# Kernel tuning notes

Hardware: AMD Instinct MI355X
Metric: run time of the kernel (lower is better)

## Reference

```python
import jax, jax.numpy as jnp
import numpy as np

B, S, H = 4, 2048, 1024
NH, HD = 16, 64
FF = 4096
EPS = 1e-5

def _ln(x, g, b):
    m = jnp.mean(x, axis=-1, keepdims=True)
    v = jnp.var(x, axis=-1, keepdims=True)
    return (x - m) * jax.lax.rsqrt(v + EPS) * g + b

def setup_inputs() -> dict:
    key = jax.random.key(0)
    ks = jax.random.split(key, 12)
    sc = 0.02
    return {
        "hidden_states": jax.random.normal(ks[0], (B, S, H), jnp.float32),
        "Wq": jax.random.normal(ks[1], (H, H), jnp.float32) * sc,
        "bq": jnp.zeros((H,), jnp.float32),
        "Wk": jax.random.normal(ks[2], (H, H), jnp.float32) * sc,
        "bk": jnp.zeros((H,), jnp.float32),
        "Wv": jax.random.normal(ks[3], (H, H), jnp.float32) * sc,
        "bv": jnp.zeros((H,), jnp.float32),
        "Wi": jax.random.normal(ks[4], (H, FF), jnp.float32) * sc,
        "bi": jnp.zeros((FF,), jnp.float32),
        "Wo": jax.random.normal(ks[5], (FF, H), jnp.float32) * sc,
        "bo": jnp.zeros((H,), jnp.float32),
        "g1": jnp.ones((H,), jnp.float32),
        "b1": jnp.zeros((H,), jnp.float32),
        "g2": jnp.ones((H,), jnp.float32),
        "b2": jnp.zeros((H,), jnp.float32),
    }

def reference(hidden_states, Wq, bq, Wk, bk, Wv, bv, Wi, bi, Wo, bo, g1, b1, g2, b2):
    x = hidden_states
    # projections -> [B, NH, S, HD]
    def split(t):
        return t.reshape(B, S, NH, HD).transpose(0, 2, 1, 3)
    q = split(x @ Wq + bq)
    k = split(x @ Wk + bk)
    v = split(x @ Wv + bv)
    scores = jnp.einsum('bhqd,bhkd->bhqk', q, k) / jnp.sqrt(jnp.float32(HD))
    probs = jax.nn.softmax(scores, axis=-1)
    ctx = jnp.einsum('bhqk,bhkd->bhqd', probs, v)
    attn_out = ctx.transpose(0, 2, 1, 3).reshape(B, S, H)
    h = _ln(x + attn_out, g1, b1)
    ffn = jax.nn.gelu(h @ Wi + bi, approximate=False) @ Wo + bo
    return _ln(h + ffn, g2, b2)
```

## Files before the change

kernel.cpp:

```cpp
#include <hip/hip_runtime.h>

#define B_  4
#define S_  2048
#define H_  1024
#define NH_ 16
#define HD_ 64
#define FF_ 4096
#define M_  (B_*S_)

typedef __bf16 bf16x8 __attribute__((ext_vector_type(8)));
typedef float  f32x4  __attribute__((ext_vector_type(4)));
typedef unsigned short ushort8v __attribute__((ext_vector_type(8)));
typedef unsigned short ushort4v __attribute__((ext_vector_type(4)));

typedef __attribute__((address_space(1))) void GVOID;
typedef __attribute__((address_space(3))) void LVOID;

__device__ __forceinline__ void g2l16(const void* g, void* l) {
  __builtin_amdgcn_global_load_lds((GVOID*)g, (LVOID*)l, 16, 0, 0);
}

#define MFMA16(a, b, c) __builtin_amdgcn_mfma_f32_16x16x32_bf16(a, b, c, 0, 0, 0)

#if __has_builtin(__builtin_amdgcn_exp2f)
#define EXP2(x) __builtin_amdgcn_exp2f(x)
#else
#define EXP2(x) exp2f(x)
#endif

__device__ __forceinline__ unsigned short f2bf(float f) {
  unsigned int u = __float_as_uint(f);
  u += 0x7fffu + ((u >> 16) & 1u);
  return (unsigned short)(u >> 16);
}
__device__ __forceinline__ float bf2f(unsigned short h) {
  return __uint_as_float(((unsigned int)h) << 16);
}

__device__ __forceinline__ float gelu_fast(float v) {
  float y = 0.7978845608f * (v + 0.044715f * v * v * v);
  float e = EXP2(y * 2.8853900818f);
  float th = 1.0f - 2.0f / (e + 1.0f);
  return 0.5f * v * (1.0f + th);
}

__device__ __forceinline__ void xcd_swz(int& bx, int& by) {
  int gx = gridDim.x;
  int flat = by * gx + bx;
  int cpx = (gx * gridDim.y) >> 3;
  int swz = (flat & 7) * cpx + (flat >> 3);
  bx = swz % gx;
  by = swz / gx;
}

__device__ __forceinline__ void xcd_swzT(int& bx, int& by) {
  int gy = gridDim.y;
  int flat = bx * gy + by;
  int cpx = (gridDim.x * gy) >> 3;
  int swz = (flat & 7) * cpx + (flat >> 3);
  by = swz % gy;
  bx = swz / gy;
}

__global__ __launch_bounds__(256) void cast_f32_bf16(const float* __restrict__ in,
                                                     unsigned short* __restrict__ out,
                                                     int n4) {
  int i = blockIdx.x * 256 + threadIdx.x;
  if (i >= n4) return;
  float4 v = reinterpret_cast<const float4*>(in)[i];
  ushort4v o;
  o[0] = f2bf(v.x); o[1] = f2bf(v.y); o[2] = f2bf(v.z); o[3] = f2bf(v.w);
  reinterpret_cast<ushort4v*>(out)[i] = o;
}

__global__ __launch_bounds__(256) void prep_weights(const float* __restrict__ Wq,
                                                    const float* __restrict__ Wk,
                                                    const float* __restrict__ Wv,
                                                    const float* __restrict__ Wi,
                                                    const float* __restrict__ Wo,
                                                    unsigned short* __restrict__ WqkvT,
                                                    unsigned short* __restrict__ WiT,
                                                    unsigned short* __restrict__ WoT) {
  __shared__ float t[32][33];
  int id = blockIdx.x;
  const float* in; unsigned short* out; int R, C, bx, by;
  if (id < 3072) {
    int seg = id >> 10, rem = id & 1023;
    in = (seg == 0) ? Wq : (seg == 1) ? Wk : Wv;
    out = WqkvT + (size_t)seg * H_ * H_;
    R = H_; C = H_;
    bx = rem & 31; by = rem >> 5;
  } else if (id < 3072 + 4096) {
    int rem = id - 3072;
    in = Wi; out = WiT; R = H_; C = FF_;
    bx = rem & 127; by = rem >> 7;
  } else {
    int rem = id - 3072 - 4096;
    in = Wo; out = WoT; R = FF_; C = H_;
    bx = rem & 31; by = rem >> 5;
  }
  bx *= 32; by *= 32;
  const int tx = threadIdx.x & 31, ty = threadIdx.x >> 5;
#pragma unroll
  for (int i = 0; i < 32; i += 8)
    t[ty + i][tx] = in[(size_t)(by + ty + i) * C + bx + tx];
  __syncthreads();
#pragma unroll
  for (int i = 0; i < 32; i += 8)
    out[(size_t)(bx + ty + i) * R + by + tx] = f2bf(t[tx][ty + i]);
}

#define ALOAD(bufv, mf, ks)                                                      \
  *reinterpret_cast<const bf16x8*>((char*)As + (bufv)*32768 + wm*16384 +         \
      ((mf)*16 + lr)*128 + (((((ks)*4 + kg)) ^ (lr & 7)) * 16))
#define BLOAD(bufv, nf, ks)                                                      \
  *reinterpret_cast<const bf16x8*>((char*)Bs + (bufv)*32768 + bh*16384 +         \
      (brow0 + (nf)*16 + lr)*128 + (((((ks)*4 + kg)) ^ (lr & 7)) * 16))

#define PH_MFMA(MF0)                                                             \
  __builtin_amdgcn_s_barrier();                                                  \
  asm volatile("s_waitcnt lgkmcnt(0)" ::: "memory");                             \
  __builtin_amdgcn_s_setprio(1);                                                 \
  _Pragma("unroll")                                                              \
  for (int nf = 0; nf < 4; ++nf) {                                               \
    acc[MF0][nf]     = MFMA16(a_[0][0], bfr[nf][0], acc[MF0][nf]);               \
    acc[MF0][nf]     = MFMA16(a_[0][1], bfr[nf][1], acc[MF0][nf]);               \
    acc[MF0 + 1][nf] = MFMA16(a_[1][0], bfr[nf][0], acc[MF0 + 1][nf]);           \
    acc[MF0 + 1][nf] = MFMA16(a_[1][1], bfr[nf][1], acc[MF0 + 1][nf]);           \
  }                                                                              \
  __builtin_amdgcn_s_setprio(0);

#define GEMM256_CORE(A_, Bt_, LDK_, NKT_, KOFF_)                                 \
  __shared__ unsigned short As[2][2][128 * 64];                                  \
  __shared__ unsigned short Bs[2][2][128 * 64];                                  \
  const int tid  = threadIdx.x;                                                  \
  const int wave = tid >> 6;                                                     \
  const int lane = tid & 63;                                                     \
  const int kg   = lane >> 4;                                                    \
  const int lr   = lane & 15;                                                    \
  const int wm   = wave >> 2;                                                    \
  const int wn   = wave & 3;                                                     \
  const int bh   = wn >> 1;                                                      \
  const int brow0 = (wn & 1) * 64;                                               \
  const int sr = lane >> 3;                                                      \
  const int sc = ((lane & 7) ^ sr) * 8;                                          \
  const unsigned short* sA = &A_[(size_t)(m0 + wave * 8 + sr) * LDK_ + KOFF_ + sc];  \
  const unsigned short* sB = &Bt_[(size_t)(n0 + wave * 8 + sr) * LDK_ + KOFF_ + sc]; \
  char* ldsA = (char*)&As[0][0][0] + wave * 1024;                                \
  char* ldsB = (char*)&Bs[0][0][0] + wave * 1024;                                \
  const size_t rkI = (size_t)64 * LDK_;                                          \
  const size_t rhK = (size_t)128 * LDK_;                                         \
  f32x4 acc[8][4] = {};                                                          \
  const int nkt = (NKT_);                                                        \
  g2l16(sA,             ldsA);                                                   \
  g2l16(sA + rkI,       ldsA + 8192);                                            \
  g2l16(sA + rhK,       ldsA + 16384);                                           \
  g2l16(sA + rhK + rkI, ldsA + 16384 + 8192);                                    \
  g2l16(sB,             ldsB);                                                   \
  g2l16(sB + rkI,       ldsB + 8192);                                            \
  g2l16(sB + rhK,       ldsB + 16384);                                           \
  g2l16(sB + rhK + rkI, ldsB + 16384 + 8192);                                    \
  g2l16(sB + 64,             ldsB + 32768);                                      \
  g2l16(sB + rkI + 64,       ldsB + 32768 + 8192);                               \
  g2l16(sB + rhK + 64,       ldsB + 32768 + 16384);                              \
  g2l16(sB + rhK + rkI + 64, ldsB + 32768 + 16384 + 8192);                       \
  asm volatile("s_waitcnt vmcnt(4)" ::: "memory");                               \
  __builtin_amdgcn_s_barrier();                                                  \
  for (int c = 0; c < nkt; ++c) {                                                \
    const int buf = c & 1;                                                       \
    const bool stgA = (c + 1 < nkt);                                             \
    const bool stgB = (c + 2 < nkt);                                             \
    const size_t kA = (size_t)(c + 1) * 64;                                      \
    const size_t kB = (size_t)(c + 2) * 64;                                      \
    bf16x8 bfr[4][2];                                                            \
    bf16x8 a_[2][2];                                                             \
    _Pragma("unroll")                                                            \
    for (int nf = 0; nf < 4; ++nf) {                                             \
      bfr[nf][0] = BLOAD(buf, nf, 0);                                            \
      bfr[nf][1] = BLOAD(buf, nf, 1);                                            \
    }                                                                            \
    a_[0][0] = ALOAD(buf, 0, 0); a_[0][1] = ALOAD(buf, 0, 1);                    \
    a_[1][0] = ALOAD(buf, 1, 0); a_[1][1] = ALOAD(buf, 1, 1);                    \
    if (stgA) {                                                                  \
      g2l16(sA + kA,       ldsA + (buf ^ 1) * 32768);                            \
      g2l16(sA + rkI + kA, ldsA + (buf ^ 1) * 32768 + 8192);                     \
    }                                                                            \
    PH_MFMA(0)                                                                   \
    __builtin_amdgcn_s_barrier();                                                \
    a_[0][0] = ALOAD(buf, 2, 0); a_[0][1] = ALOAD(buf, 2, 1);                    \
    a_[1][0] = ALOAD(buf, 3, 0); a_[1][1] = ALOAD(buf, 3, 1);                    \
    if (stgA) {                                                                  \
      g2l16(sA + rhK + kA,       ldsA + (buf ^ 1) * 32768 + 16384);              \
      g2l16(sA + rhK + rkI + kA, ldsA + (buf ^ 1) * 32768 + 16384 + 8192);       \
    }                                                                            \
    PH_MFMA(2)                                                                   \
    __builtin_amdgcn_s_barrier();                                                \
    a_[0][0] = ALOAD(buf, 4, 0); a_[0][1] = ALOAD(buf, 4, 1);                    \
    a_[1][0] = ALOAD(buf, 5, 0); a_[1][1] = ALOAD(buf, 5, 1);                    \
    if (stgB) {                                                                  \
      g2l16(sB + kB,       ldsB + buf * 32768);                                  \
      g2l16(sB + rkI + kB, ldsB + buf * 32768 + 8192);                           \
    }                                                                            \
    PH_MFMA(4)                                                                   \
    __builtin_amdgcn_s_barrier();                                                \
    a_[0][0] = ALOAD(buf, 6, 0); a_[0][1] = ALOAD(buf, 6, 1);                    \
    a_[1][0] = ALOAD(buf, 7, 0); a_[1][1] = ALOAD(buf, 7, 1);                    \
    if (stgB) {                                                                  \
      g2l16(sB + rhK + kB,       ldsB + buf * 32768 + 16384);                    \
      g2l16(sB + rhK + rkI + kB, ldsB + buf * 32768 + 16384 + 8192);             \
    }                                                                            \
    PH_MFMA(6)                                                                   \
    if (c < nkt - 2)       asm volatile("s_waitcnt vmcnt(4)" ::: "memory");      \
    else if (c == nkt - 2) asm volatile("s_waitcnt vmcnt(0)" ::: "memory");      \
    __builtin_amdgcn_s_barrier();                                                \
  }

template<int ACT, int OUT_F32>
__global__ __launch_bounds__(512, 1) void gemm256_tn(const unsigned short* __restrict__ A,
                                                     const unsigned short* __restrict__ Bt,
                                                     const float* __restrict__ bias,
                                                     void* __restrict__ C,
                                                     int M, int N, int K) {
  int bx = blockIdx.x, by = blockIdx.y;
  xcd_swzT(bx, by);
  const int z = blockIdx.z;
  const int Klen = K / gridDim.z;
  const int Koff = z * Klen;
  const float* biasEff = (z == 0) ? bias : nullptr;
  const int m0 = bx * 256;
  const int n0 = by * 256;
  GEMM256_CORE(A, Bt, K, Klen >> 6, Koff)

  float* Cf = (float*)C + (size_t)z * M * N;
#pragma unroll
  for (int mf = 0; mf < 8; ++mf) {
#pragma unroll
    for (int nf = 0; nf < 4; ++nf) {
      int col = n0 + wn * 64 + nf * 16 + lr;
      float bc = biasEff ? biasEff[col] : 0.0f;
#pragma unroll
      for (int r = 0; r < 4; ++r) {
        int row = m0 + wm * 128 + mf * 16 + kg * 4 + r;
        float v = acc[mf][nf][r] + bc;
        if (ACT == 1) v = gelu_fast(v);
        if (OUT_F32) Cf[(size_t)row * N + col] = v;
        else reinterpret_cast<unsigned short*>(C)[(size_t)row * N + col] = f2bf(v);
      }
    }
  }
}

__global__ __launch_bounds__(512, 1) void gemm256_qkv(const unsigned short* __restrict__ A,
                                                      const unsigned short* __restrict__ Bt,
                                                      const float* __restrict__ bq,
                                                      const float* __restrict__ bk,
                                                      const float* __restrict__ bv,
                                                      unsigned short* __restrict__ qb,
                                                      unsigned short* __restrict__ kb,
                                                      unsigned short* __restrict__ vt,
                                                      float qscale) {
  int bx = blockIdx.x, by = blockIdx.y;
  xcd_swzT(bx, by);
  const int m0 = bx * 256;
  const int n0 = by * 256;
  GEMM256_CORE(A, Bt, H_, H_ >> 6, 0)

#pragma unroll
  for (int mf = 0; mf < 8; ++mf) {
#pragma unroll
    for (int nf = 0; nf < 4; ++nf) {
      int colb = n0 + wn * 64 + nf * 16;
      int col  = colb + lr;
      int seg  = colb >> 10;
      int row0 = m0 + wm * 128 + mf * 16 + kg * 4;
      if (seg == 0) {
        float bc = bq[col];
#pragma unroll
        for (int r = 0; r < 4; ++r)
          qb[(size_t)(row0 + r) * H_ + col] = f2bf((acc[mf][nf][r] + bc) * qscale);
      } else if (seg == 1) {
        float bc = bk[col - 1024];
#pragma unroll
        for (int r = 0; r < 4; ++r)
          kb[(size_t)(row0 + r) * H_ + col - 1024] = f2bf(acc[mf][nf][r] + bc);
      } else {
        float bc = bv[col - 2048];
        ushort4v o;
#pragma unroll
        for (int r = 0; r < 4; ++r) o[r] = f2bf(acc[mf][nf][r] + bc);
        *reinterpret_cast<ushort4v*>(&vt[(size_t)(col - 2048) * M_ + row0]) = o;
      }
    }
  }
}

__global__ __launch_bounds__(512) void attn_fwd(const unsigned short* __restrict__ Q,
                                                const unsigned short* __restrict__ Kb,
                                                const unsigned short* __restrict__ VT,
                                                unsigned short* __restrict__ O) {
  __shared__ unsigned short Ks[2][64 * 64];
  __shared__ unsigned short Vs[2][64 * 64];
  __shared__ __bf16 Ps[8][32 * 64];

  const int tid  = threadIdx.x;
  const int wave = tid >> 6;
  const int lane = tid & 63;
  const int kg   = lane >> 4;
  const int lr   = lane & 15;
  int bx = blockIdx.x, by = blockIdx.y;
  xcd_swz(bx, by);
  const int b  = by >> 4;
  const int h  = by & 15;
  const size_t rowbase = (size_t)b * S_;
  const int hcol = h * 64;
  const int bcol0 = b * S_;
  const int q0 = bx * 256 + wave * 32;

  const int rT = wave * 8 + (lane >> 3);
  const int ce = ((lane & 7) * 8) ^ (((lane >> 3) & 7) << 3);
  const int fswz = (lr & 7) << 3;

  bf16x8 qf[2][2];
#pragma unroll
  for (int sub = 0; sub < 2; ++sub)
#pragma unroll
    for (int d = 0; d < 2; ++d)
      qf[sub][d] = *reinterpret_cast<const bf16x8*>(
          &Q[(rowbase + q0 + sub * 16 + lr) * H_ + hcol + d * 32 + kg * 8]);

  bf16x8 ones;
#pragma unroll
  for (int i = 0; i < 8; ++i) ones[i] = (__bf16)1.0f;

  const f32x4 cinit = {-8.0f, -8.0f, -8.0f, -8.0f};

  f32x4 ctx[2][4] = {};
  f32x4 lsum[2] = {};

  auto stage = [&](int kt, int buf) {
    g2l16(&Kb[(rowbase + kt * 64 + rT) * H_ + hcol + ce], &Ks[buf][wave * 512]);
    g2l16(&VT[(size_t)(hcol + rT) * M_ + bcol0 + kt * 64 + ce], &Vs[buf][wave * 512]);
  };

  stage(0, 0);
  __syncthreads();

  const int NT = S_ / 64;
  for (int kt = 0; kt < NT; ++kt) {
    const int cur = kt & 1;
    if (kt + 1 < NT) stage(kt + 1, cur ^ 1);

    f32x4 s0[4], s1[4];
    __builtin_amdgcn_s_setprio(1);
#pragma unroll
    for (int nf = 0; nf < 4; ++nf) {
      int row = nf * 16 + lr;
      bf16x8 kf0 = *reinterpret_cast<const bf16x8*>(&Ks[cur][row * 64 + ((kg * 8) ^ fswz)]);
      bf16x8 kf1 = *reinterpret_cast<const bf16x8*>(&Ks[cur][row * 64 + ((32 + kg * 8) ^ fswz)]);
      f32x4 z0 = cinit, z1 = cinit;
      z0 = MFMA16(qf[0][0], kf0, z0);
      z0 = MFMA16(qf[0][1], kf1, z0);
      z1 = MFMA16(qf[1][0], kf0, z1);
      z1 = MFMA16(qf[1][1], kf1, z1);
      s0[nf] = z0;
      s1[nf] = z1;
    }
    __builtin_amdgcn_s_setprio(0);

#pragma unroll
    for (int nf = 0; nf < 4; ++nf)
#pragma unroll
      for (int r = 0; r < 4; ++r) {
        int row = kg * 4 + r;
        Ps[wave][row * 64 + ((nf * 16 + lr) ^ ((row & 7) << 3))] =
            (__bf16)EXP2(s0[nf][r]);
        Ps[wave][(16 + row) * 64 + ((nf * 16 + lr) ^ ((row & 7) << 3))] =
            (__bf16)EXP2(s1[nf][r]);
      }
    bf16x8 p00 = *reinterpret_cast<const bf16x8*>(
        &Ps[wave][lr * 64 + ((kg ^ (lr & 7)) << 3)]);
    bf16x8 p01 = *reinterpret_cast<const bf16x8*>(
        &Ps[wave][lr * 64 + (((4 + kg) ^ (lr & 7)) << 3)]);
    bf16x8 p10 = *reinterpret_cast<const bf16x8*>(
        &Ps[wave][(16 + lr) * 64 + ((kg ^ (lr & 7)) << 3)]);
    bf16x8 p11 = *reinterpret_cast<const bf16x8*>(
        &Ps[wave][(16 + lr) * 64 + (((4 + kg) ^ (lr & 7)) << 3)]);

    __builtin_amdgcn_s_setprio(1);
#pragma unroll
    for (int df = 0; df < 4; ++df) {
      int row = df * 16 + lr;
      bf16x8 vf0 = *reinterpret_cast<const bf16x8*>(&Vs[cur][row * 64 + ((kg * 8) ^ fswz)]);
      bf16x8 vf1 = *reinterpret_cast<const bf16x8*>(&Vs[cur][row * 64 + ((32 + kg * 8) ^ fswz)]);
      ctx[0][df] = MFMA16(p00, vf0, ctx[0][df]);
      ctx[0][df] = MFMA16(p01, vf1, ctx[0][df]);
      ctx[1][df] = MFMA16(p10, vf0, ctx[1][df]);
      ctx[1][df] = MFMA16(p11, vf1, ctx[1][df]);
    }
    lsum[0] = MFMA16(p00, ones, lsum[0]);
    lsum[0] = MFMA16(p01, ones, lsum[0]);
    lsum[1] = MFMA16(p10, ones, lsum[1]);
    lsum[1] = MFMA16(p11, ones, lsum[1]);
    __builtin_amdgcn_s_setprio(0);

    __syncthreads();
  }

#pragma unroll
  for (int sub = 0; sub < 2; ++sub)
#pragma unroll
    for (int r = 0; r < 4; ++r) {
      float rl = 1.0f / lsum[sub][r];
#pragma unroll
      for (int df = 0; df < 4; ++df) {
        float v = ctx[sub][df][r] * rl;
        O[(rowbase + q0 + sub * 16 + kg * 4 + r) * H_ + hcol + df * 16 + lr] = f2bf(v);
      }
    }
}

template<int IN2_BF16, int WRITE_BF16>
__global__ __launch_bounds__(256) void add_ln(const float* __restrict__ X,
                                              const void* __restrict__ Y,
                                              const float* __restrict__ g,
                                              const float* __restrict__ beta,
                                              float* __restrict__ outF,
                                              unsigned short* __restrict__ outB) {
  const int row = blockIdx.x;
  const int tid = threadIdx.x;
  const int wave = tid >> 6, lane = tid & 63;
  __shared__ float red[8];

  const size_t base = (size_t)row * H_ + tid * 4;
  float4 xv = *reinterpret_cast<const float4*>(&X[base]);
  float vals[4] = {xv.x, xv.y, xv.z, xv.w};
  if (IN2_BF16) {
    ushort4v yv = *reinterpret_cast<const ushort4v*>(
        &reinterpret_cast<const unsigned short*>(Y)[base]);
#pragma unroll
    for (int i = 0; i < 4; ++i) vals[i] += bf2f(yv[i]);
  } else {
    float4 yv = *reinterpret_cast<const float4*>(&reinterpret_cast<const float*>(Y)[base]);
    vals[0] += yv.x; vals[1] += yv.y; vals[2] += yv.z; vals[3] += yv.w;
  }
  float s = 0.0f, s2 = 0.0f;
#pragma unroll
  for (int i = 0; i < 4; ++i) { s += vals[i]; s2 += vals[i] * vals[i]; }
#pragma unroll
  for (int off = 32; off; off >>= 1) { s += __shfl_xor(s, off); s2 += __shfl_xor(s2, off); }
  if (lane == 0) { red[wave * 2] = s; red[wave * 2 + 1] = s2; }
  __syncthreads();
  s  = red[0] + red[2] + red[4] + red[6];
  s2 = red[1] + red[3] + red[5] + red[7];
  float mean = s * (1.0f / H_);
  float var  = s2 * (1.0f / H_) - mean * mean;
  float rstd = rsqrtf(var + 1e-5f);

  float4 gv = *reinterpret_cast<const float4*>(&g[tid * 4]);
  float4 bv = *reinterpret_cast<const float4*>(&beta[tid * 4]);
  float gs[4] = {gv.x, gv.y, gv.z, gv.w};
  float bs[4] = {bv.x, bv.y, bv.z, bv.w};
  float4 of;
  ushort4v ob;
#pragma unroll
  for (int i = 0; i < 4; ++i) {
    float v = (vals[i] - mean) * rstd * gs[i] + bs[i];
    ((float*)&of)[i] = v;
    ob[i] = f2bf(v);
  }
  if (outF) *reinterpret_cast<float4*>(&outF[base]) = of;
  if (WRITE_BF16) *reinterpret_cast<ushort4v*>(&outB[base]) = ob;
}

__global__ __launch_bounds__(256) void add_ln3(const float* __restrict__ X,
                                               const float* __restrict__ Y0,
                                               const float* __restrict__ Y1,
                                               const float* __restrict__ g,
                                               const float* __restrict__ beta,
                                               float* __restrict__ outF) {
  const int row = blockIdx.x;
  const int tid = threadIdx.x;
  const int wave = tid >> 6, lane = tid & 63;
  __shared__ float red[8];

  const size_t base = (size_t)row * H_ + tid * 4;
  float4 xv = *reinterpret_cast<const float4*>(&X[base]);
  float4 y0 = *reinterpret_cast<const float4*>(&Y0[base]);
  float4 y1 = *reinterpret_cast<const float4*>(&Y1[base]);
  float vals[4] = {xv.x + y0.x + y1.x, xv.y + y0.y + y1.y,
                   xv.z + y0.z + y1.z, xv.w + y0.w + y1.w};
  float s = 0.0f, s2 = 0.0f;
#pragma unroll
  for (int i = 0; i < 4; ++i) { s += vals[i]; s2 += vals[i] * vals[i]; }
#pragma unroll
  for (int off = 32; off; off >>= 1) { s += __shfl_xor(s, off); s2 += __shfl_xor(s2, off); }
  if (lane == 0) { red[wave * 2] = s; red[wave * 2 + 1] = s2; }
  __syncthreads();
  s  = red[0] + red[2] + red[4] + red[6];
  s2 = red[1] + red[3] + red[5] + red[7];
  float mean = s * (1.0f / H_);
  float var  = s2 * (1.0f / H_) - mean * mean;
  float rstd = rsqrtf(var + 1e-5f);

  float4 gv = *reinterpret_cast<const float4*>(&g[tid * 4]);
  float4 bv = *reinterpret_cast<const float4*>(&beta[tid * 4]);
  float4 of;
  of.x = (vals[0] - mean) * rstd * gv.x + bv.x;
  of.y = (vals[1] - mean) * rstd * gv.y + bv.y;
  of.z = (vals[2] - mean) * rstd * gv.z + bv.z;
  of.w = (vals[3] - mean) * rstd * gv.w + bv.w;
  *reinterpret_cast<float4*>(&outF[base]) = of;
}

extern "C" void kernel_launch(void* const* d_in, const int* in_sizes, int n_in,
                              void* d_out, int out_size, void* d_ws, size_t ws_size,
                              hipStream_t stream) {
  const float* x  = (const float*)d_in[0];
  const float* Wq = (const float*)d_in[1];
  const float* bq = (const float*)d_in[2];
  const float* Wk = (const float*)d_in[3];
  const float* bk = (const float*)d_in[4];
  const float* Wv = (const float*)d_in[5];
  const float* bv = (const float*)d_in[6];
  const float* Wi = (const float*)d_in[7];
  const float* bi = (const float*)d_in[8];
  const float* Wo = (const float*)d_in[9];
  const float* bo = (const float*)d_in[10];
  const float* g1 = (const float*)d_in[11];
  const float* b1 = (const float*)d_in[12];
  const float* g2 = (const float*)d_in[13];
  const float* b2 = (const float*)d_in[14];

  unsigned char* ws = (unsigned char*)d_ws;
  size_t off = 0;
  auto alloc = [&](size_t bytes) { size_t o = off; off += (bytes + 255) & ~(size_t)255; return o; };

  unsigned short* WqkvT = (unsigned short*)(ws + alloc((size_t)3 * H_ * H_ * 2));
  unsigned short* WiT   = (unsigned short*)(ws + alloc((size_t)H_ * FF_ * 2));
  unsigned short* WoT   = (unsigned short*)(ws + alloc((size_t)FF_ * H_ * 2));
  float*          hf    = (float*)(ws + alloc((size_t)M_ * H_ * 4));
  unsigned short* hb    = (unsigned short*)(ws + alloc((size_t)M_ * H_ * 2));
  unsigned short* f1    = (unsigned short*)(ws + alloc((size_t)M_ * FF_ * 2));
  unsigned short* xb    = (unsigned short*)(ws + alloc((size_t)M_ * H_ * 2));
  unsigned short* qb    = (unsigned short*)(ws + alloc((size_t)M_ * H_ * 2));
  unsigned short* kb    = (unsigned short*)(ws + alloc((size_t)M_ * H_ * 2));
  unsigned short* vt    = (unsigned short*)(ws + alloc((size_t)M_ * H_ * 2));
  unsigned short* ao    = (unsigned short*)(ws + alloc((size_t)M_ * H_ * 2));
  float*          f2p   = (float*)xb;

  {
    int n4 = (int)((size_t)M_ * H_ / 4);
    cast_f32_bf16<<<(n4 + 255) / 256, 256, 0, stream>>>(x, xb, n4);
  }
  prep_weights<<<3072 + 4096 + 4096, 256, 0, stream>>>(Wq, Wk, Wv, Wi, Wo,
                                                       WqkvT, WiT, WoT);

  const float QSCALE = 0.125f * 1.44269504088896340736f;

  gemm256_qkv<<<dim3(M_ / 256, 3072 / 256), 512, 0, stream>>>(xb, WqkvT, bq, bk, bv,
                                                              qb, kb, vt, QSCALE);

  attn_fwd<<<dim3(S_ / 256, B_ * NH_), 512, 0, stream>>>(qb, kb, vt, ao);

  add_ln<1, 1><<<M_, 256, 0, stream>>>(x, ao, g1, b1, hf, hb);

  gemm256_tn<1, 0><<<dim3(M_ / 256, FF_ / 256), 512, 0, stream>>>(hb, WiT, bi, f1, M_, FF_, H_);
  gemm256_tn<0, 1><<<dim3(M_ / 256, H_ / 256, 2), 512, 0, stream>>>(f1, WoT, bo, f2p, M_, H_, FF_);

  add_ln3<<<M_, 256, 0, stream>>>(hf, f2p, f2p + (size_t)M_ * H_, g2, b2, (float*)d_out);
}
```

Measured before the change: 433.5 us.

## Compute transposed scores in attention to keep P in registers; drop fp32 LN1 output

The attention kernel now computes S^T by swapping MFMA operands. Each lane then holds probabilities along keys, and the P fragments for the PV MFMA are assembled with cross-lane shuffles instead of a round trip through LDS. Row sums come from in-register adds plus shuffles rather than extra MFMAs against a ones vector, and the output is written as packed 4-element vectors. Separately, the first LayerNorm writes only a bf16 output, and the second residual reads that bf16 tensor, removing an fp32 M×H write and read at some cost in residual precision.

```diff
diff --git a/kernel.cpp b/kernel.cpp
--- a/kernel.cpp
+++ b/kernel.cpp
@@ -12,6 +12,7 @@
 typedef float  f32x4  __attribute__((ext_vector_type(4)));
 typedef unsigned short ushort8v __attribute__((ext_vector_type(8)));
 typedef unsigned short ushort4v __attribute__((ext_vector_type(4)));
+typedef unsigned int   uint4v   __attribute__((ext_vector_type(4)));
 
 typedef __attribute__((address_space(1))) void GVOID;
 typedef __attribute__((address_space(3))) void LVOID;
@@ -300,7 +301,6 @@
                                                 unsigned short* __restrict__ O) {
   __shared__ unsigned short Ks[2][64 * 64];
   __shared__ unsigned short Vs[2][64 * 64];
-  __shared__ __bf16 Ps[8][32 * 64];
 
   const int tid  = threadIdx.x;
   const int wave = tid >> 6;
@@ -318,7 +318,6 @@
 
   const int rT = wave * 8 + (lane >> 3);
   const int ce = ((lane & 7) * 8) ^ (((lane >> 3) & 7) << 3);
-  const int fswz = (lr & 7) << 3;
 
   bf16x8 qf[2][2];
 #pragma unroll
@@ -328,14 +327,12 @@
       qf[sub][d] = *reinterpret_cast<const bf16x8*>(
           &Q[(rowbase + q0 + sub * 16 + lr) * H_ + hcol + d * 32 + kg * 8]);
 
-  bf16x8 ones;
-#pragma unroll
-  for (int i = 0; i < 8; ++i) ones[i] = (__bf16)1.0f;
-
   const f32x4 cinit = {-8.0f, -8.0f, -8.0f, -8.0f};
 
-  f32x4 ctx[2][4] = {};
-  f32x4 lsum[2] = {};
+  f32x4 ctxT[2][4] = {};
+  float lsumS[2] = {0.0f, 0.0f};
+
+  const int srcA = lr + ((kg & 1) << 5);
 
   auto stage = [&](int kt, int buf) {
     g2l16(&Kb[(rowbase + kt * 64 + rT) * H_ + hcol + ce], &Ks[buf][wave * 512]);
@@ -350,82 +347,101 @@
     const int cur = kt & 1;
     if (kt + 1 < NT) stage(kt + 1, cur ^ 1);
 
-    f32x4 s0[4], s1[4];
+    f32x4 sT[2][4];
     __builtin_amdgcn_s_setprio(1);
 #pragma unroll
     for (int nf = 0; nf < 4; ++nf) {
       int row = nf * 16 + lr;
-      bf16x8 kf0 = *reinterpret_cast<const bf16x8*>(&Ks[cur][row * 64 + ((kg * 8) ^ fswz)]);
-      bf16x8 kf1 = *reinterpret_cast<const bf16x8*>(&Ks[cur][row * 64 + ((32 + kg * 8) ^ fswz)]);
+      bf16x8 kf0 = *reinterpret_cast<const bf16x8*>(
+          &Ks[cur][row * 64 + (((kg ^ (lr & 7))) << 3)]);
+      bf16x8 kf1 = *reinterpret_cast<const bf16x8*>(
+          &Ks[cur][row * 64 + ((((4 + kg) ^ (lr & 7))) << 3)]);
       f32x4 z0 = cinit, z1 = cinit;
-      z0 = MFMA16(qf[0][0], kf0, z0);
-      z0 = MFMA16(qf[0][1], kf1, z0);
-      z1 = MFMA16(qf[1][0], kf0, z1);
-      z1 = MFMA16(qf[1][1], kf1, z1);
-      s0[nf] = z0;
-      s1[nf] = z1;
+      z0 = MFMA16(kf0, qf[0][0], z0);
+      z0 = MFMA16(kf1, qf[0][1], z0);
+      z1 = MFMA16(kf0, qf[1][0], z1);
+      z1 = MFMA16(kf1, qf[1][1], z1);
+      sT[0][nf] = z0;
+      sT[1][nf] = z1;
     }
     __builtin_amdgcn_s_setprio(0);
 
-#pragma unroll
-    for (int nf = 0; nf < 4; ++nf)
-#pragma unroll
-      for (int r = 0; r < 4; ++r) {
-        int row = kg * 4 + r;
-        Ps[wave][row * 64 + ((nf * 16 + lr) ^ ((row & 7) << 3))] =
-            (__bf16)EXP2(s0[nf][r]);
-        Ps[wave][(16 + row) * 64 + ((nf * 16 + lr) ^ ((row & 7) << 3))] =
-            (__bf16)EXP2(s1[nf][r]);
+    bf16x8 pf[2][2];
+#pragma unroll
+    for (int sub = 0; sub < 2; ++sub) {
+      unsigned p01[4], p23[4];
+      float rs = 0.0f;
+#pragma unroll
+      for (int nf = 0; nf < 4; ++nf) {
+        float e0 = EXP2(sT[sub][nf][0]);
+        float e1 = EXP2(sT[sub][nf][1]);
+        float e2 = EXP2(sT[sub][nf][2]);
+        float e3 = EXP2(sT[sub][nf][3]);
+        rs += (e0 + e1) + (e2 + e3);
+        p01[nf] = (unsigned)f2bf(e0) | ((unsigned)f2bf(e1) << 16);
+        p23[nf] = (unsigned)f2bf(e2) | ((unsigned)f2bf(e3) << 16);
       }
-    bf16x8 p00 = *reinterpret_cast<const bf16x8*>(
-        &Ps[wave][lr * 64 + ((kg ^ (lr & 7)) << 3)]);
-    bf16x8 p01 = *reinterpret_cast<const bf16x8*>(
-        &Ps[wave][lr * 64 + (((4 + kg) ^ (lr & 7)) << 3)]);
-    bf16x8 p10 = *reinterpret_cast<const bf16x8*>(
-        &Ps[wave][(16 + lr) * 64 + ((kg ^ (lr & 7)) << 3)]);
-    bf16x8 p11 = *reinterpret_cast<const bf16x8*>(
-        &Ps[wave][(16 + lr) * 64 + (((4 + kg) ^ (lr & 7)) << 3)]);
+      rs += __shfl_xor(rs, 16);
+      rs += __shfl_xor(rs, 32);
+      lsumS[sub] = (kt == 0) ? rs : (lsumS[sub] + rs);
+
+#pragma unroll
+      for (int ks = 0; ks < 2; ++ks) {
+        unsigned lo0 = (unsigned)__shfl((int)p01[2 * ks],     srcA);
+        unsigned lo1 = (unsigned)__shfl((int)p01[2 * ks + 1], srcA);
+        unsigned m0  = (unsigned)__shfl((int)p23[2 * ks],     srcA);
+        unsigned m1  = (unsigned)__shfl((int)p23[2 * ks + 1], srcA);
+        unsigned hi0 = (unsigned)__shfl((int)p01[2 * ks],     srcA + 16);
+        unsigned hi1 = (unsigned)__shfl((int)p01[2 * ks + 1], srcA + 16);
+        unsigned n0  = (unsigned)__shfl((int)p23[2 * ks],     srcA + 16);
+        unsigned n1  = (unsigned)__shfl((int)p23[2 * ks + 1], srcA + 16);
+        bool hi = (kg & 2);
+        uint4v w;
+        w[0] = hi ? lo1 : lo0;
+        w[1] = hi ? m1  : m0;
+        w[2] = hi ? hi1 : hi0;
+        w[3] = hi ? n1  : n0;
+        pf[sub][ks] = __builtin_bit_cast(bf16x8, w);
+      }
+    }
 
     __builtin_amdgcn_s_setprio(1);
 #pragma unroll
     for (int df = 0; df < 4; ++df) {
       int row = df * 16 + lr;
-      bf16x8 vf0 = *reinterpret_cast<const bf16x8*>(&Vs[cur][row * 64 + ((kg * 8) ^ fswz)]);
-      bf16x8 vf1 = *reinterpret_cast<const bf16x8*>(&Vs[cur][row * 64 + ((32 + kg * 8) ^ fswz)]);
-      ctx[0][df] = MFMA16(p00, vf0, ctx[0][df]);
-      ctx[0][df] = MFMA16(p01, vf1, ctx[0][df]);
-      ctx[1][df] = MFMA16(p10, vf0, ctx[1][df]);
-      ctx[1][df] = MFMA16(p11, vf1, ctx[1][df]);
+      bf16x8 vf0 = *reinterpret_cast<const bf16x8*>(
+          &Vs[cur][row * 64 + (((kg ^ (lr & 7))) << 3)]);
+      bf16x8 vf1 = *reinterpret_cast<const bf16x8*>(
+          &Vs[cur][row * 64 + ((((4 + kg) ^ (lr & 7))) << 3)]);
+      ctxT[0][df] = MFMA16(vf0, pf[0][0], ctxT[0][df]);
+      ctxT[0][df] = MFMA16(vf1, pf[0][1], ctxT[0][df]);
+      ctxT[1][df] = MFMA16(vf0, pf[1][0], ctxT[1][df]);
+      ctxT[1][df] = MFMA16(vf1, pf[1][1], ctxT[1][df]);
     }
-    lsum[0] = MFMA16(p00, ones, lsum[0]);
-    lsum[0] = MFMA16(p01, ones, lsum[0]);
-    lsum[1] = MFMA16(p10, ones, lsum[1]);
-    lsum[1] = MFMA16(p11, ones, lsum[1]);
     __builtin_amdgcn_s_setprio(0);
 
     __syncthreads();
   }
 
 #pragma unroll
-  for (int sub = 0; sub < 2; ++sub)
-#pragma unroll
-    for (int r = 0; r < 4; ++r) {
-      float rl = 1.0f / lsum[sub][r];
-#pragma unroll
-      for (int df = 0; df < 4; ++df) {
-        float v = ctx[sub][df][r] * rl;
-        O[(rowbase + q0 + sub * 16 + kg * 4 + r) * H_ + hcol + df * 16 + lr] = f2bf(v);
-      }
+  for (int sub = 0; sub < 2; ++sub) {
+    float rl = 1.0f / lsumS[sub];
+#pragma unroll
+    for (int df = 0; df < 4; ++df) {
+      ushort4v o;
+#pragma unroll
+      for (int r = 0; r < 4; ++r) o[r] = f2bf(ctxT[sub][df][r] * rl);
+      *reinterpret_cast<ushort4v*>(
+          &O[(rowbase + q0 + sub * 16 + lr) * H_ + hcol + df * 16 + kg * 4]) = o;
     }
-}
-
-template<int IN2_BF16, int WRITE_BF16>
-__global__ __launch_bounds__(256) void add_ln(const float* __restrict__ X,
-                                              const void* __restrict__ Y,
-                                              const float* __restrict__ g,
-                                              const float* __restrict__ beta,
-                                              float* __restrict__ outF,
-                                              unsigned short* __restrict__ outB) {
+  }
+}
+
+__global__ __launch_bounds__(256) void add_ln_b(const float* __restrict__ X,
+                                                const unsigned short* __restrict__ Y,
+                                                const float* __restrict__ g,
+                                                const float* __restrict__ beta,
+                                                unsigned short* __restrict__ outB) {
   const int row = blockIdx.x;
   const int tid = threadIdx.x;
   const int wave = tid >> 6, lane = tid & 63;
@@ -433,16 +449,9 @@
 
   const size_t base = (size_t)row * H_ + tid * 4;
   float4 xv = *reinterpret_cast<const float4*>(&X[base]);
-  float vals[4] = {xv.x, xv.y, xv.z, xv.w};
-  if (IN2_BF16) {
-    ushort4v yv = *reinterpret_cast<const ushort4v*>(
-        &reinterpret_cast<const unsigned short*>(Y)[base]);
-#pragma unroll
-    for (int i = 0; i < 4; ++i) vals[i] += bf2f(yv[i]);
-  } else {
-    float4 yv = *reinterpret_cast<const float4*>(&reinterpret_cast<const float*>(Y)[base]);
-    vals[0] += yv.x; vals[1] += yv.y; vals[2] += yv.z; vals[3] += yv.w;
-  }
+  ushort4v yv = *reinterpret_cast<const ushort4v*>(&Y[base]);
+  float vals[4] = {xv.x + bf2f(yv[0]), xv.y + bf2f(yv[1]),
+                   xv.z + bf2f(yv[2]), xv.w + bf2f(yv[3])};
   float s = 0.0f, s2 = 0.0f;
 #pragma unroll
   for (int i = 0; i < 4; ++i) { s += vals[i]; s2 += vals[i] * vals[i]; }
@@ -460,19 +469,14 @@
   float4 bv = *reinterpret_cast<const float4*>(&beta[tid * 4]);
   float gs[4] = {gv.x, gv.y, gv.z, gv.w};
   float bs[4] = {bv.x, bv.y, bv.z, bv.w};
-  float4 of;
   ushort4v ob;
 #pragma unroll
-  for (int i = 0; i < 4; ++i) {
-    float v = (vals[i] - mean) * rstd * gs[i] + bs[i];
-    ((float*)&of)[i] = v;
-    ob[i] = f2bf(v);
-  }
-  if (outF) *reinterpret_cast<float4*>(&outF[base]) = of;
-  if (WRITE_BF16) *reinterpret_cast<ushort4v*>(&outB[base]) = ob;
-}
-
-__global__ __launch_bounds__(256) void add_ln3(const float* __restrict__ X,
+  for (int i = 0; i < 4; ++i)
+    ob[i] = f2bf((vals[i] - mean) * rstd * gs[i] + bs[i]);
+  *reinterpret_cast<ushort4v*>(&outB[base]) = ob;
+}
+
+__global__ __launch_bounds__(256) void add_ln3(const unsigned short* __restrict__ X,
                                                const float* __restrict__ Y0,
                                                const float* __restrict__ Y1,
                                                const float* __restrict__ g,
@@ -484,11 +488,11 @@
   __shared__ float red[8];
 
   const size_t base = (size_t)row * H_ + tid * 4;
-  float4 xv = *reinterpret_cast<const float4*>(&X[base]);
+  ushort4v xv = *reinterpret_cast<const ushort4v*>(&X[base]);
   float4 y0 = *reinterpret_cast<const float4*>(&Y0[base]);
   float4 y1 = *reinterpret_cast<const float4*>(&Y1[base]);
-  float vals[4] = {xv.x + y0.x + y1.x, xv.y + y0.y + y1.y,
-                   xv.z + y0.z + y1.z, xv.w + y0.w + y1.w};
+  float vals[4] = {bf2f(xv[0]) + y0.x + y1.x, bf2f(xv[1]) + y0.y + y1.y,
+                   bf2f(xv[2]) + y0.z + y1.z, bf2f(xv[3]) + y0.w + y1.w};
   float s = 0.0f, s2 = 0.0f;
 #pragma unroll
   for (int i = 0; i < 4; ++i) { s += vals[i]; s2 += vals[i] * vals[i]; }
@@ -538,7 +542,6 @@
   unsigned short* WqkvT = (unsigned short*)(ws + alloc((size_t)3 * H_ * H_ * 2));
   unsigned short* WiT   = (unsigned short*)(ws + alloc((size_t)H_ * FF_ * 2));
   unsigned short* WoT   = (unsigned short*)(ws + alloc((size_t)FF_ * H_ * 2));
-  float*          hf    = (float*)(ws + alloc((size_t)M_ * H_ * 4));
   unsigned short* hb    = (unsigned short*)(ws + alloc((size_t)M_ * H_ * 2));
   unsigned short* f1    = (unsigned short*)(ws + alloc((size_t)M_ * FF_ * 2));
   unsigned short* xb    = (unsigned short*)(ws + alloc((size_t)M_ * H_ * 2));
@@ -562,10 +565,10 @@
 
   attn_fwd<<<dim3(S_ / 256, B_ * NH_), 512, 0, stream>>>(qb, kb, vt, ao);
 
-  add_ln<1, 1><<<M_, 256, 0, stream>>>(x, ao, g1, b1, hf, hb);
+  add_ln_b<<<M_, 256, 0, stream>>>(x, ao, g1, b1, hb);
 
   gemm256_tn<1, 0><<<dim3(M_ / 256, FF_ / 256), 512, 0, stream>>>(hb, WiT, bi, f1, M_, FF_, H_);
   gemm256_tn<0, 1><<<dim3(M_ / 256, H_ / 256, 2), 512, 0, stream>>>(f1, WoT, bo, f2p, M_, H_, FF_);
 
-  add_ln3<<<M_, 256, 0, stream>>>(hf, f2p, f2p + (size_t)M_ * H_, g2, b2, (float*)d_out);
-}
+  add_ln3<<<M_, 256, 0, stream>>>(hb, f2p, f2p + (size_t)M_ * H_, g2, b2, (float*)d_out);
+}
```

Result: no change. 434.8 us (+0.3%).
